# Kernel optimization log

Hardware: AMD Instinct MI355X
Metric: run time of the kernel (lower is better)

## Reference

```python
import jax, jax.numpy as jnp
import numpy as np

B = 256
D = 512
C = 100000
S = 30.0
M = 0.5
COS_M = float(np.cos(M))
SIN_M = float(np.sin(M))
TH = float(np.cos(np.pi - M))
MM = float(np.sin(np.pi - M) * M)


def setup_inputs() -> dict:
    key = jax.random.key(0)
    k1, k2, k3, k4 = jax.random.split(key, 4)
    image_emb = jax.random.normal(k1, (B, D), dtype=jnp.float32)
    profile_emb = jax.random.normal(k2, (B, D), dtype=jnp.float32)
    # xavier_uniform_ for weight [C, D]: bound = sqrt(6/(C+D))
    bound = float(np.sqrt(6.0 / (C + D)))
    weight = jax.random.uniform(k3, (C, D), dtype=jnp.float32, minval=-bound, maxval=bound)
    label = jax.random.randint(k4, (B,), 0, C, dtype=jnp.int64)
    return {"image_emb": image_emb, "profile_emb": profile_emb, "weight": weight, "label": label}


def reference(image_emb, profile_emb, weight, label):
    emb = jnp.concatenate([image_emb, profile_emb], axis=0)          # [2B, D]
    lab = jnp.tile(label, (2,))                                      # [2B]
    emb_n = emb / jnp.linalg.norm(emb, axis=1, keepdims=True)
    w_n = weight / jnp.linalg.norm(weight, axis=1, keepdims=True)
    cosine = jnp.einsum('nd,cd->nc', emb_n, w_n)                     # [2B, C]
    sine = jnp.sqrt(jnp.clip(1.0 - cosine * cosine, 0.0, 1.0))
    phi = cosine * COS_M - sine * SIN_M
    phi = jnp.where(cosine > TH, phi, cosine - MM)                   # easy_margin=False
    one_hot = jnp.arange(cosine.shape[1])[None, :] == lab[:, None]   # [2B, C] bool
    logits = S * jnp.where(one_hot, phi, cosine)
    logp = jax.nn.log_softmax(logits, axis=1)
    nll = -jnp.take_along_axis(logp, lab[:, None], axis=1)[:, 0]
    return jnp.mean(nll)
```

## Files before the change

### kernel.cpp

```cpp
#include <hip/hip_runtime.h>

#define S_SCALE 30.0f
#define COS_M 0.8775825618903728f
#define SIN_M 0.479425538604203f
#define TH_C (-0.8775825618903728f)
#define MM_C 0.2397127693021015f

#define BD 512
#define DD 512
#define CC 100000
#define NCB2 782
#define LASTB2 781
#define NPART 1564
#define CPAD 100096
#define NWB 12512

typedef __bf16 bf16x8 __attribute__((ext_vector_type(8)));
typedef __bf16 bf16x4 __attribute__((ext_vector_type(4)));
typedef float  f32x4  __attribute__((ext_vector_type(4)));

#define AS1 __attribute__((address_space(1)))
#define AS3 __attribute__((address_space(3)))

__global__ __launch_bounds__(256) void k_prep(const float* __restrict__ img,
                                              const float* __restrict__ prof,
                                              const float* __restrict__ W,
                                              const int* __restrict__ lab,
                                              __bf16* __restrict__ At,
                                              float* __restrict__ sphi,
                                              float* __restrict__ scos,
                                              __bf16* __restrict__ Wt,
                                              float* __restrict__ csqg,
                                              int* __restrict__ cnt) {
    const int t = threadIdx.x;

    if (blockIdx.x < 128) {
        const int wave = t >> 6, l = t & 63;
        if (blockIdx.x == 0 && t == 0) cnt[0] = 0;
        const int row = blockIdx.x * 4 + wave;
        const float* src = (row < 256) ? (img + (size_t)row * DD)
                                       : (prof + (size_t)(row - 256) * DD);
        float4 v0 = ((const float4*)src)[l * 2];
        float4 v1 = ((const float4*)src)[l * 2 + 1];
        float s = v0.x * v0.x + v0.y * v0.y + v0.z * v0.z + v0.w * v0.w
                + v1.x * v1.x + v1.y * v1.y + v1.z * v1.z + v1.w * v1.w;
        #pragma unroll
        for (int o = 1; o < 64; o <<= 1) s += __shfl_xor(s, o);
        float r = rsqrtf(s);
        bf16x8 a;
        a[0] = (__bf16)(v0.x * r); a[1] = (__bf16)(v0.y * r);
        a[2] = (__bf16)(v0.z * r); a[3] = (__bf16)(v0.w * r);
        a[4] = (__bf16)(v1.x * r); a[5] = (__bf16)(v1.y * r);
        a[6] = (__bf16)(v1.z * r); a[7] = (__bf16)(v1.w * r);
        *(bf16x8*)(At + (size_t)(l >> 2) * (BD * 32) + row * 32 + (l & 3) * 8) = a;

        const int c = lab[row & 255];
        const float4* wc = (const float4*)(W + (size_t)c * DD);
        float4 w0 = wc[l * 2], w1 = wc[l * 2 + 1];
        float wb0 = (float)(__bf16)w0.x, wb1 = (float)(__bf16)w0.y;
        float wb2 = (float)(__bf16)w0.z, wb3 = (float)(__bf16)w0.w;
        float wb4 = (float)(__bf16)w1.x, wb5 = (float)(__bf16)w1.y;
        float wb6 = (float)(__bf16)w1.z, wb7 = (float)(__bf16)w1.w;
        float dot = (float)a[0] * wb0 + (float)a[1] * wb1 + (float)a[2] * wb2
                  + (float)a[3] * wb3 + (float)a[4] * wb4 + (float)a[5] * wb5
                  + (float)a[6] * wb6 + (float)a[7] * wb7;
        float wsq = wb0 * wb0 + wb1 * wb1 + wb2 * wb2 + wb3 * wb3
                  + wb4 * wb4 + wb5 * wb5 + wb6 * wb6 + wb7 * wb7;
        #pragma unroll
        for (int o = 1; o < 64; o <<= 1) { dot += __shfl_xor(dot, o); wsq += __shfl_xor(wsq, o); }
        if (l == 0) {
            float cs = dot * rsqrtf(wsq);
            float sn = sqrtf(fmaxf(0.f, fminf(1.f, 1.f - cs * cs)));
            float phi = cs * COS_M - sn * SIN_M;
            if (!(cs > TH_C)) phi = cs - MM_C;
            sphi[row] = S_SCALE * phi;
            scos[row] = S_SCALE * cs;
        }
        return;
    }

    const int wb  = blockIdx.x - 128;
    const int row = wb * 8 + (t >> 5);
    const int g   = t & 31;
    float sq = 0.f;
    bf16x4 ob[4];
    if (row < CC) {
        const float4* src = (const float4*)(W + (size_t)row * DD);
        #pragma unroll
        for (int i = 0; i < 4; ++i) {
            float4 v = src[g + 32 * i];
            bf16x4 b;
            b[0] = (__bf16)v.x; b[1] = (__bf16)v.y;
            b[2] = (__bf16)v.z; b[3] = (__bf16)v.w;
            float f;
            f = (float)b[0]; sq += f * f; f = (float)b[1]; sq += f * f;
            f = (float)b[2]; sq += f * f; f = (float)b[3]; sq += f * f;
            ob[i] = b;
        }
    } else {
        #pragma unroll
        for (int i = 0; i < 4; ++i)
            ob[i] = bf16x4{(__bf16)0.f, (__bf16)0.f, (__bf16)0.f, (__bf16)0.f};
    }
    #pragma unroll
    for (int o = 1; o < 32; o <<= 1) sq += __shfl_xor(sq, o);
    bf16x4* dst = (bf16x4*)(Wt + (size_t)row * DD);
    #pragma unroll
    for (int i = 0; i < 4; ++i) dst[g + 32 * i] = ob[i];
    if (g == 0) csqg[row] = (row < CC) ? sq : 1.0f;
}

__global__ __launch_bounds__(256, 2) void k_gemm(const __bf16* __restrict__ At,
                                                 const __bf16* __restrict__ Wt,
                                                 const float* __restrict__ csqg,
                                                 float* __restrict__ part) {
    __shared__ __bf16 As[2][256 * 32];
    __shared__ __bf16 Bs[2][128 * 32];

    const int t = threadIdx.x;
    const int bid = blockIdx.x;
    const int rb = bid & 1;
    const int cb = bid >> 1;
    const int wave = t >> 6, lane = t & 63, q = lane >> 4, m16 = lane & 15;
    const int wr = wave >> 1, wc = wave & 1;

    const int frag_off = m16 * 32 + ((q ^ ((m16 >> 1) & 3)) << 3);
    const int srcswz = ((t >> 2) << 6) + ((((t & 3) ^ ((t >> 3) & 3))) << 4);
    const char* abase = (const char*)At + (size_t)rb * 16384 + srcswz;

    const int bcol = t >> 2, bs = t & 3;
    const int bswz = (bs ^ ((bcol >> 1) & 3)) << 4;
    const char* bsrc0 = (const char*)Wt + (size_t)(cb * 128 + bcol) * 1024 + bswz;
    const char* bsrc1 = (const char*)Wt + (size_t)(cb * 128 + 64 + bcol) * 1024 + bswz;

    f32x4 acc[8][4] = {};

#define GLDS_A(kt, buf)                                                                 \
    {                                                                                   \
        _Pragma("unroll")                                                               \
        for (int p = 0; p < 4; ++p)                                                     \
            __builtin_amdgcn_global_load_lds(                                           \
                (AS1 void*)(abase + (size_t)(kt) * 32768 + p * 4096),                   \
                (AS3 void*)((char*)(&As[buf][0]) + p * 4096 + wave * 1024),             \
                16, 0, 0);                                                              \
    }
#define GLDS_B(kt, buf)                                                                 \
    {                                                                                   \
        __builtin_amdgcn_global_load_lds(                                               \
            (AS1 void*)(bsrc0 + (kt) * 64),                                             \
            (AS3 void*)((char*)(&Bs[buf][0]) + wave * 1024), 16, 0, 0);                 \
        __builtin_amdgcn_global_load_lds(                                               \
            (AS1 void*)(bsrc1 + (kt) * 64),                                             \
            (AS3 void*)((char*)(&Bs[buf][0]) + 4096 + wave * 1024), 16, 0, 0);          \
    }

    GLDS_A(0, 0);
    GLDS_B(0, 0);

    #pragma unroll
    for (int kt = 0; kt < 16; ++kt) {
        __syncthreads();
        if (kt < 15) {
            GLDS_A(kt + 1, (kt + 1) & 1);
            GLDS_B(kt + 1, (kt + 1) & 1);
        }
        bf16x8 bfrag[4], afrag[8];
        #pragma unroll
        for (int j = 0; j < 4; ++j)
            bfrag[j] = *(const bf16x8*)(&Bs[kt & 1][wc * 2048 + j * 512 + frag_off]);
        #pragma unroll
        for (int i = 0; i < 8; ++i)
            afrag[i] = *(const bf16x8*)(&As[kt & 1][wr * 4096 + i * 512 + frag_off]);
        #pragma unroll
        for (int i = 0; i < 8; ++i) {
            #pragma unroll
            for (int j = 0; j < 4; ++j)
                acc[i][j] = __builtin_amdgcn_mfma_f32_16x16x32_bf16(
                    afrag[i], bfrag[j], acc[i][j], 0, 0, 0);
        }
    }

    const bool lastb = (cb == LASTB2);
    float inv[4]; bool val[4];
    #pragma unroll
    for (int j = 0; j < 4; ++j) {
        int ct = wc * 64 + j * 16 + m16;
        val[j] = (!lastb) || (ct < 32);
        inv[j] = rsqrtf(csqg[cb * 128 + ct]) * S_SCALE;
    }
    #pragma unroll
    for (int i = 0; i < 8; ++i) {
        #pragma unroll
        for (int r = 0; r < 4; ++r) {
            float e = 0.f;
            #pragma unroll
            for (int j = 0; j < 4; ++j)
                if (val[j]) e += __expf(acc[i][j][r] * inv[j]);
            e += __shfl_xor(e, 1);
            e += __shfl_xor(e, 2);
            e += __shfl_xor(e, 4);
            e += __shfl_xor(e, 8);
            if (m16 == 0)
                part[((size_t)cb * 2 + wc) * BD + rb * 256 + wr * 128 + i * 16 + q * 4 + r] = e;
        }
    }
#undef GLDS_A
#undef GLDS_B
}

__global__ __launch_bounds__(256) void k_reduce(const float* __restrict__ part,
                                                const float* __restrict__ sphi,
                                                const float* __restrict__ scos,
                                                float* __restrict__ rowpart,
                                                int* __restrict__ cnt,
                                                float* __restrict__ out) {
    const int b = blockIdx.x;
    const int rg = b >> 5, cp = b & 31;
    const int t = threadIdx.x;
    const int rl = t & 63, ph = t >> 6;
    const int r0 = rg * 64;
    float s = 0.f;
    for (int c0 = cp * 4 + ph; c0 < NPART; c0 += 128)
        s += part[(size_t)c0 * BD + r0 + rl];
    __shared__ float buf[256];
    buf[t] = s;
    __syncthreads();
    if (t < 64)
        rowpart[(size_t)cp * BD + r0 + t] = buf[t] + buf[t + 64] + buf[t + 128] + buf[t + 192];

    __threadfence();
    __syncthreads();
    __shared__ int lastf;
    if (t == 0) lastf = (atomicAdd(cnt, 1) == 255) ? 1 : 0;
    __syncthreads();
    if (!lastf) return;
    __threadfence();

    float a = 0.f;
    for (int r = t; r < BD; r += 256) {
        float total = 0.f;
        #pragma unroll
        for (int c = 0; c < 32; ++c)
            total += rowpart[(size_t)c * BD + r];
        float lse = logf(total);
        float sp = sphi[r], sc = scos[r];
        float corr = log1pf(__expf(sp - lse) - __expf(sc - lse));
        a += lse + corr - sp;
    }
    #pragma unroll
    for (int o = 1; o < 64; o <<= 1) a += __shfl_xor(a, o);
    __shared__ float wsum[4];
    if ((t & 63) == 0) wsum[t >> 6] = a;
    __syncthreads();
    if (t == 0) out[0] = (wsum[0] + wsum[1] + wsum[2] + wsum[3]) * (1.0f / 512.0f);
}

extern "C" void kernel_launch(void* const* d_in, const int* in_sizes, int n_in,
                              void* d_out, int out_size, void* d_ws, size_t ws_size,
                              hipStream_t stream) {
    const float* img  = (const float*)d_in[0];
    const float* prof = (const float*)d_in[1];
    const float* W    = (const float*)d_in[2];
    const int*   lab  = (const int*)d_in[3];

    char* ws = (char*)d_ws;
    __bf16* At     = (__bf16*)ws;
    float* sphi    = (float*)(ws + 524288);
    float* scos    = (float*)(ws + 526336);
    float* part    = (float*)(ws + 528384);
    float* rowpart = (float*)(ws + 3731456);
    float* csqg    = (float*)(ws + 3796992);
    int*   cnt     = (int*)(ws + 4197376);
    __bf16* Wt     = (__bf16*)(ws + 4198400);

    k_prep<<<128 + NWB, 256, 0, stream>>>(img, prof, W, lab, At, sphi, scos, Wt, csqg, cnt);
    k_gemm<<<2 * NCB2, 256, 0, stream>>>(At, Wt, csqg, part);
    k_reduce<<<256, 256, 0, stream>>>(part, sphi, scos, rowpart, cnt, (float*)d_out);
}
```

Measured before the change: 402.6 us.

## Triple-buffer GEMM loads, remap blocks across XCDs, split prep kernel

The GEMM main loop moves from a double-buffered LDS pipeline to a triple-buffered one that prefetches two K-tiles ahead. It replaces __syncthreads with explicit vmcnt waits plus s_barrier, and adds sched_barrier and setprio hints around the MFMA block. Block IDs are remapped so that neighbouring column blocks land on the same XCD, which is meant to improve L2 locality for the shared A tiles. The fused prep kernel is split into separate weight-conversion and activation-normalisation launches; this adds a launch and raises LDS use per block, which may lower occupancy.

```diff
diff --git a/kernel.cpp b/kernel.cpp
--- a/kernel.cpp
+++ b/kernel.cpp
@@ -22,65 +22,63 @@
 #define AS1 __attribute__((address_space(1)))
 #define AS3 __attribute__((address_space(3)))
 
-__global__ __launch_bounds__(256) void k_prep(const float* __restrict__ img,
-                                              const float* __restrict__ prof,
-                                              const float* __restrict__ W,
-                                              const int* __restrict__ lab,
-                                              __bf16* __restrict__ At,
-                                              float* __restrict__ sphi,
-                                              float* __restrict__ scos,
-                                              __bf16* __restrict__ Wt,
-                                              float* __restrict__ csqg,
-                                              int* __restrict__ cnt) {
-    const int t = threadIdx.x;
-
-    if (blockIdx.x < 128) {
-        const int wave = t >> 6, l = t & 63;
-        if (blockIdx.x == 0 && t == 0) cnt[0] = 0;
-        const int row = blockIdx.x * 4 + wave;
-        const float* src = (row < 256) ? (img + (size_t)row * DD)
-                                       : (prof + (size_t)(row - 256) * DD);
-        float4 v0 = ((const float4*)src)[l * 2];
-        float4 v1 = ((const float4*)src)[l * 2 + 1];
-        float s = v0.x * v0.x + v0.y * v0.y + v0.z * v0.z + v0.w * v0.w
-                + v1.x * v1.x + v1.y * v1.y + v1.z * v1.z + v1.w * v1.w;
-        #pragma unroll
-        for (int o = 1; o < 64; o <<= 1) s += __shfl_xor(s, o);
-        float r = rsqrtf(s);
-        bf16x8 a;
-        a[0] = (__bf16)(v0.x * r); a[1] = (__bf16)(v0.y * r);
-        a[2] = (__bf16)(v0.z * r); a[3] = (__bf16)(v0.w * r);
-        a[4] = (__bf16)(v1.x * r); a[5] = (__bf16)(v1.y * r);
-        a[6] = (__bf16)(v1.z * r); a[7] = (__bf16)(v1.w * r);
-        *(bf16x8*)(At + (size_t)(l >> 2) * (BD * 32) + row * 32 + (l & 3) * 8) = a;
-
-        const int c = lab[row & 255];
-        const float4* wc = (const float4*)(W + (size_t)c * DD);
-        float4 w0 = wc[l * 2], w1 = wc[l * 2 + 1];
-        float wb0 = (float)(__bf16)w0.x, wb1 = (float)(__bf16)w0.y;
-        float wb2 = (float)(__bf16)w0.z, wb3 = (float)(__bf16)w0.w;
-        float wb4 = (float)(__bf16)w1.x, wb5 = (float)(__bf16)w1.y;
-        float wb6 = (float)(__bf16)w1.z, wb7 = (float)(__bf16)w1.w;
-        float dot = (float)a[0] * wb0 + (float)a[1] * wb1 + (float)a[2] * wb2
-                  + (float)a[3] * wb3 + (float)a[4] * wb4 + (float)a[5] * wb5
-                  + (float)a[6] * wb6 + (float)a[7] * wb7;
-        float wsq = wb0 * wb0 + wb1 * wb1 + wb2 * wb2 + wb3 * wb3
-                  + wb4 * wb4 + wb5 * wb5 + wb6 * wb6 + wb7 * wb7;
-        #pragma unroll
-        for (int o = 1; o < 64; o <<= 1) { dot += __shfl_xor(dot, o); wsq += __shfl_xor(wsq, o); }
-        if (l == 0) {
-            float cs = dot * rsqrtf(wsq);
-            float sn = sqrtf(fmaxf(0.f, fminf(1.f, 1.f - cs * cs)));
-            float phi = cs * COS_M - sn * SIN_M;
-            if (!(cs > TH_C)) phi = cs - MM_C;
-            sphi[row] = S_SCALE * phi;
-            scos[row] = S_SCALE * cs;
-        }
-        return;
-    }
-
-    const int wb  = blockIdx.x - 128;
-    const int row = wb * 8 + (t >> 5);
+__global__ __launch_bounds__(256) void k_prep_a(const float* __restrict__ img,
+                                                const float* __restrict__ prof,
+                                                const float* __restrict__ W,
+                                                const int* __restrict__ lab,
+                                                __bf16* __restrict__ At,
+                                                float* __restrict__ sphi,
+                                                float* __restrict__ scos,
+                                                int* __restrict__ cnt) {
+    const int t = threadIdx.x;
+    const int wave = t >> 6, l = t & 63;
+    if (blockIdx.x == 0 && t == 0) cnt[0] = 0;
+    const int row = blockIdx.x * 4 + wave;
+    const float* src = (row < 256) ? (img + (size_t)row * DD)
+                                   : (prof + (size_t)(row - 256) * DD);
+    float4 v0 = ((const float4*)src)[l * 2];
+    float4 v1 = ((const float4*)src)[l * 2 + 1];
+    float s = v0.x * v0.x + v0.y * v0.y + v0.z * v0.z + v0.w * v0.w
+            + v1.x * v1.x + v1.y * v1.y + v1.z * v1.z + v1.w * v1.w;
+    #pragma unroll
+    for (int o = 1; o < 64; o <<= 1) s += __shfl_xor(s, o);
+    float r = rsqrtf(s);
+    bf16x8 a;
+    a[0] = (__bf16)(v0.x * r); a[1] = (__bf16)(v0.y * r);
+    a[2] = (__bf16)(v0.z * r); a[3] = (__bf16)(v0.w * r);
+    a[4] = (__bf16)(v1.x * r); a[5] = (__bf16)(v1.y * r);
+    a[6] = (__bf16)(v1.z * r); a[7] = (__bf16)(v1.w * r);
+    *(bf16x8*)(At + (size_t)(l >> 2) * (BD * 32) + row * 32 + (l & 3) * 8) = a;
+
+    const int c = lab[row & 255];
+    const float4* wc = (const float4*)(W + (size_t)c * DD);
+    float4 w0 = wc[l * 2], w1 = wc[l * 2 + 1];
+    float wb0 = (float)(__bf16)w0.x, wb1 = (float)(__bf16)w0.y;
+    float wb2 = (float)(__bf16)w0.z, wb3 = (float)(__bf16)w0.w;
+    float wb4 = (float)(__bf16)w1.x, wb5 = (float)(__bf16)w1.y;
+    float wb6 = (float)(__bf16)w1.z, wb7 = (float)(__bf16)w1.w;
+    float dot = (float)a[0] * wb0 + (float)a[1] * wb1 + (float)a[2] * wb2
+              + (float)a[3] * wb3 + (float)a[4] * wb4 + (float)a[5] * wb5
+              + (float)a[6] * wb6 + (float)a[7] * wb7;
+    float wsq = wb0 * wb0 + wb1 * wb1 + wb2 * wb2 + wb3 * wb3
+              + wb4 * wb4 + wb5 * wb5 + wb6 * wb6 + wb7 * wb7;
+    #pragma unroll
+    for (int o = 1; o < 64; o <<= 1) { dot += __shfl_xor(dot, o); wsq += __shfl_xor(wsq, o); }
+    if (l == 0) {
+        float cs = dot * rsqrtf(wsq);
+        float sn = sqrtf(fmaxf(0.f, fminf(1.f, 1.f - cs * cs)));
+        float phi = cs * COS_M - sn * SIN_M;
+        if (!(cs > TH_C)) phi = cs - MM_C;
+        sphi[row] = S_SCALE * phi;
+        scos[row] = S_SCALE * cs;
+    }
+}
+
+__global__ __launch_bounds__(256) void k_prep_w(const float* __restrict__ W,
+                                                __bf16* __restrict__ Wt,
+                                                float* __restrict__ csqg) {
+    const int t = threadIdx.x;
+    const int row = blockIdx.x * 8 + (t >> 5);
     const int g   = t & 31;
     float sq = 0.f;
     bf16x4 ob[4];
@@ -114,13 +112,15 @@
                                                  const __bf16* __restrict__ Wt,
                                                  const float* __restrict__ csqg,
                                                  float* __restrict__ part) {
-    __shared__ __bf16 As[2][256 * 32];
-    __shared__ __bf16 Bs[2][128 * 32];
-
-    const int t = threadIdx.x;
-    const int bid = blockIdx.x;
-    const int rb = bid & 1;
-    const int cb = bid >> 1;
+    __shared__ __bf16 As[3][256 * 32];
+    __shared__ __bf16 Bs[3][128 * 32];
+
+    const int t = threadIdx.x;
+    const int orig = blockIdx.x;
+    const int xcd = orig & 7, loc = orig >> 3;
+    const int wgid = (xcd < 4 ? xcd * 196 : 784 + (xcd - 4) * 195) + loc;
+    const int rb = wgid & 1;
+    const int cb = wgid >> 1;
     const int wave = t >> 6, lane = t & 63, q = lane >> 4, m16 = lane & 15;
     const int wr = wave >> 1, wc = wave & 1;
 
@@ -153,32 +153,44 @@
             (AS1 void*)(bsrc1 + (kt) * 64),                                             \
             (AS3 void*)((char*)(&Bs[buf][0]) + 4096 + wave * 1024), 16, 0, 0);          \
     }
-
-    GLDS_A(0, 0);
-    GLDS_B(0, 0);
-
-    #pragma unroll
-    for (int kt = 0; kt < 16; ++kt) {
-        __syncthreads();
-        if (kt < 15) {
-            GLDS_A(kt + 1, (kt + 1) & 1);
-            GLDS_B(kt + 1, (kt + 1) & 1);
-        }
-        bf16x8 bfrag[4], afrag[8];
-        #pragma unroll
-        for (int j = 0; j < 4; ++j)
-            bfrag[j] = *(const bf16x8*)(&Bs[kt & 1][wc * 2048 + j * 512 + frag_off]);
-        #pragma unroll
-        for (int i = 0; i < 8; ++i)
-            afrag[i] = *(const bf16x8*)(&As[kt & 1][wr * 4096 + i * 512 + frag_off]);
-        #pragma unroll
-        for (int i = 0; i < 8; ++i) {
-            #pragma unroll
-            for (int j = 0; j < 4; ++j)
-                acc[i][j] = __builtin_amdgcn_mfma_f32_16x16x32_bf16(
-                    afrag[i], bfrag[j], acc[i][j], 0, 0, 0);
-        }
-    }
+#define SB() __builtin_amdgcn_sched_barrier(0)
+
+#define ITER(kt, VM)                                                                    \
+    {                                                                                   \
+        asm volatile("s_waitcnt vmcnt(" #VM ")" ::: "memory");                          \
+        __builtin_amdgcn_s_barrier();                                                   \
+        SB();                                                                           \
+        if ((kt) + 2 <= 15) {                                                           \
+            GLDS_A((kt) + 2, ((kt) + 2) % 3);                                           \
+            GLDS_B((kt) + 2, ((kt) + 2) % 3);                                           \
+        }                                                                               \
+        SB();                                                                           \
+        bf16x8 bfrag[4], afrag[8];                                                      \
+        _Pragma("unroll")                                                               \
+        for (int j = 0; j < 4; ++j)                                                     \
+            bfrag[j] = *(const bf16x8*)(&Bs[(kt) % 3][wc * 2048 + j * 512 + frag_off]); \
+        _Pragma("unroll")                                                               \
+        for (int i = 0; i < 8; ++i)                                                     \
+            afrag[i] = *(const bf16x8*)(&As[(kt) % 3][wr * 4096 + i * 512 + frag_off]); \
+        __builtin_amdgcn_s_setprio(1);                                                  \
+        _Pragma("unroll")                                                               \
+        for (int i = 0; i < 8; ++i) {                                                   \
+            _Pragma("unroll")                                                           \
+            for (int j = 0; j < 4; ++j)                                                 \
+                acc[i][j] = __builtin_amdgcn_mfma_f32_16x16x32_bf16(                    \
+                    afrag[i], bfrag[j], acc[i][j], 0, 0, 0);                            \
+        }                                                                               \
+        __builtin_amdgcn_s_setprio(0);                                                  \
+    }
+
+    GLDS_A(0, 0); GLDS_B(0, 0);
+    GLDS_A(1, 1); GLDS_B(1, 1);
+    SB();
+
+    ITER(0, 6);  ITER(1, 6);  ITER(2, 6);  ITER(3, 6);
+    ITER(4, 6);  ITER(5, 6);  ITER(6, 6);  ITER(7, 6);
+    ITER(8, 6);  ITER(9, 6);  ITER(10, 6); ITER(11, 6);
+    ITER(12, 6); ITER(13, 6); ITER(14, 6); ITER(15, 0);
 
     const bool lastb = (cb == LASTB2);
     float inv[4]; bool val[4];
@@ -206,6 +218,8 @@
     }
 #undef GLDS_A
 #undef GLDS_B
+#undef SB
+#undef ITER
 }
 
 __global__ __launch_bounds__(256) void k_reduce(const float* __restrict__ part,
@@ -273,7 +287,8 @@
     int*   cnt     = (int*)(ws + 4197376);
     __bf16* Wt     = (__bf16*)(ws + 4198400);
 
-    k_prep<<<128 + NWB, 256, 0, stream>>>(img, prof, W, lab, At, sphi, scos, Wt, csqg, cnt);
+    k_prep_w<<<NWB, 256, 0, stream>>>(W, Wt, csqg);
+    k_prep_a<<<128, 256, 0, stream>>>(img, prof, W, lab, At, sphi, scos, cnt);
     k_gemm<<<2 * NCB2, 256, 0, stream>>>(At, Wt, csqg, part);
     k_reduce<<<256, 256, 0, stream>>>(part, sphi, scos, rowpart, cnt, (float*)d_out);
 }
```

Measured after the change: 404.2 us. About the same (+0.4%).
